# Performance work log

Measured on AMD Instinct MI355X. Metric: run time of the kernel, lower is better.

## Reference

```python
import jax, jax.numpy as jnp
import numpy as np

B, S, L, DM, DP, H, HT, NO = 1, 64, 256, 256, 128, 8, 4, 32
EPS = 1e-5


def _lin(key, din, dout):
    k1, k2 = jax.random.split(key)
    s = 1.0 / np.sqrt(din)
    w = jax.random.uniform(k1, (din, dout), minval=-s, maxval=s, dtype=jnp.float32)
    b = jax.random.uniform(k2, (dout,), minval=-s, maxval=s, dtype=jnp.float32)
    return w, b


def setup_inputs() -> dict:
    key = jax.random.key(0)
    ks = jax.random.split(key, 16)
    inp = {}
    inp['msa'] = jax.random.normal(ks[0], (B, S, L, DM), dtype=jnp.float32)
    inp['pair'] = jax.random.normal(ks[1], (B, L, L, DP), dtype=jnp.float32)
    # row attention
    inp['row_norm_g'] = jnp.ones((DM,), jnp.float32); inp['row_norm_b'] = jnp.zeros((DM,), jnp.float32)
    inp['row_qkv_w'], inp['row_qkv_b'] = _lin(ks[2], DM, 3 * DM)
    inp['row_out_w'], inp['row_out_b'] = _lin(ks[3], DM, DM)
    # column attention
    inp['col_norm_g'] = jnp.ones((DM,), jnp.float32); inp['col_norm_b'] = jnp.zeros((DM,), jnp.float32)
    inp['col_qkv_w'], inp['col_qkv_b'] = _lin(ks[4], DM, 3 * DM)
    inp['col_out_w'], inp['col_out_b'] = _lin(ks[5], DM, DM)
    inp['ff_norm_g'] = jnp.ones((DM,), jnp.float32); inp['ff_norm_b'] = jnp.zeros((DM,), jnp.float32)
    inp['ff_w1'], inp['ff_b1'] = _lin(ks[6], DM, 4 * DM)
    inp['ff_w2'], inp['ff_b2'] = _lin(ks[7], 4 * DM, DM)
    # outer product mean
    inp['op_norm_g'] = jnp.ones((DM,), jnp.float32); inp['op_norm_b'] = jnp.zeros((DM,), jnp.float32)
    inp['op_a_w'], inp['op_a_b'] = _lin(ks[8], DM, NO)
    inp['op_b_w'], inp['op_b_b'] = _lin(ks[9], DM, NO)
    inp['op_out_w'], inp['op_out_b'] = _lin(ks[10], NO * NO, DP)
    # triangle attention
    inp['tri_norm_g'] = jnp.ones((DP,), jnp.float32); inp['tri_norm_b'] = jnp.zeros((DP,), jnp.float32)
    inp['tri_qkv_w'], inp['tri_qkv_b'] = _lin(ks[11], DP, 3 * DP)
    inp['tri_out_w'], inp['tri_out_b'] = _lin(ks[12], DP, DP)
    return inp


def layer_norm(x, g, b):
    m = jnp.mean(x, axis=-1, keepdims=True)
    v = jnp.mean(jnp.square(x - m), axis=-1, keepdims=True)
    return (x - m) * jax.lax.rsqrt(v + EPS) * g + b


def mha(x, qkv_w, qkv_b, out_w, out_b, n_heads):
    # x: (..., n, d); attention over axis n. Dropout is eval-mode (identity).
    *lead, n, d = x.shape
    hd = d // n_heads
    qkv = x @ qkv_w + qkv_b
    q, k, v = jnp.split(qkv, 3, axis=-1)
    q = q.reshape(*lead, n, n_heads, hd)
    k = k.reshape(*lead, n, n_heads, hd)
    v = v.reshape(*lead, n, n_heads, hd)
    attn = jnp.einsum('...ihd,...jhd->...hij', q, k) * (hd ** -0.5)
    attn = jnp.clip(attn, -50.0, 50.0)
    attn = jax.nn.softmax(attn, axis=-1)
    out = jnp.einsum('...hij,...jhd->...ihd', attn, v).reshape(*lead, n, d)
    return out @ out_w + out_b


def reference(msa, pair,
              row_norm_g, row_norm_b, row_qkv_w, row_qkv_b, row_out_w, row_out_b,
              col_norm_g, col_norm_b, col_qkv_w, col_qkv_b, col_out_w, col_out_b,
              ff_norm_g, ff_norm_b, ff_w1, ff_b1, ff_w2, ff_b2,
              op_norm_g, op_norm_b, op_a_w, op_a_b, op_b_w, op_b_b, op_out_w, op_out_b,
              tri_norm_g, tri_norm_b, tri_qkv_w, tri_qkv_b, tri_out_w, tri_out_b):
    # row attention over seq_len axis
    msa = msa + mha(layer_norm(msa, row_norm_g, row_norm_b),
                    row_qkv_w, row_qkv_b, row_out_w, row_out_b, H)
    # column attention: transpose (b s n d) -> (b n s d), attend over n_seqs
    msa_t = jnp.swapaxes(msa, 1, 2)
    msa_t = msa_t + mha(layer_norm(msa_t, col_norm_g, col_norm_b),
                        col_qkv_w, col_qkv_b, col_out_w, col_out_b, H)
    msa = jnp.swapaxes(msa_t, 1, 2)
    # feed-forward
    h = layer_norm(msa, ff_norm_g, ff_norm_b)
    msa = msa + (jax.nn.relu(h @ ff_w1 + ff_b1) @ ff_w2 + ff_b2)
    # outer product mean: msa -> pair update
    m = layer_norm(msa, op_norm_g, op_norm_b)
    a = m @ op_a_w + op_a_b   # (b, s, L, NO)
    b_ = m @ op_b_w + op_b_b  # (b, s, L, NO)
    n_seqs = msa.shape[1]
    outer = jnp.einsum('bsic,bsjd->bijcd', a, b_) / float(n_seqs)  # (b, L, L, NO, NO)
    bsz, Ld = outer.shape[0], outer.shape[1]
    pair = pair + outer.reshape(bsz, Ld, Ld, NO * NO) @ op_out_w + op_out_b
    # triangle attention (row-wise attention over last L axis, 4 heads)
    pn = layer_norm(pair, tri_norm_g, tri_norm_b)
    pair = pair + mha(pn, tri_qkv_w, tri_qkv_b, tri_out_w, tri_out_b, HT)
    return msa, pair
```

## Files before the change

### kernel.cpp

```cpp
#include <hip/hip_runtime.h>
#include <hip/hip_bf16.h>


#define S_ 64
#define L_ 256
#define DM_ 256
#define DP_ 128
#define H_ 8
#define HT_ 4
#define NO_ 32

typedef __hip_bfloat16 bf16;
typedef short short4s __attribute__((ext_vector_type(4)));
typedef short short8 __attribute__((ext_vector_type(8)));
typedef float floatx4 __attribute__((ext_vector_type(4)));

__device__ __forceinline__ short f2bfs(float x) {
  union { float f; unsigned u; } v;
  v.f = x;
  unsigned r = (v.u + 0x7fffu + ((v.u >> 16) & 1u)) >> 16;
  return (short)r;
}

__global__ void k_ln(const float* __restrict__ src, bf16* __restrict__ dst,
                     const float* __restrict__ g, const float* __restrict__ bta, int D) {
  int row = blockIdx.x * 4 + (threadIdx.x >> 6);
  const float* x = src + (size_t)row * D;
  bf16* y = dst + (size_t)row * D;
  int t = threadIdx.x & 63;
  float v[4];
  int cnt = 0;
  float sum = 0.f;
  for (int e = t; e < D; e += 64) { float xv = x[e]; v[cnt++] = xv; sum += xv; }
  #pragma unroll
  for (int o = 32; o; o >>= 1) sum += __shfl_down(sum, o);
  sum = __shfl(sum, 0);
  float mean = sum / D;
  float var = 0.f;
  for (int k = 0; k < cnt; k++) { float d = v[k] - mean; var += d * d; }
  #pragma unroll
  for (int o = 32; o; o >>= 1) var += __shfl_down(var, o);
  var = __shfl(var, 0);
  float rstd = rsqrtf(var / D + 1e-5f);
  cnt = 0;
  for (int e = t; e < D; e += 64)
    y[e] = __float2bfloat16((v[cnt++] - mean) * rstd * g[e] + bta[e]);
}

struct WtJob { const float* W; bf16* Wt; int K; int N; int nblk; };
struct WtJobs { WtJob j[10]; };

__global__ void k_wt_all(WtJobs jobs) {
  __shared__ float tile[32][33];
  int b = blockIdx.x;
  int ji = 0;
  while (ji < 9 && b >= jobs.j[ji].nblk) { b -= jobs.j[ji].nblk; ji++; }
  const float* W = jobs.j[ji].W;
  bf16* Wt = jobs.j[ji].Wt;
  int K = jobs.j[ji].K, N = jobs.j[ji].N;
  int kt = K >> 5;
  int k0 = (b % kt) * 32, n0 = (b / kt) * 32;
  int tid = threadIdx.x;
  for (int e = tid; e < 1024; e += 256) {
    int r = e >> 5, c = e & 31;
    tile[r][c] = W[(size_t)(k0 + r) * N + (n0 + c)];
  }
  __syncthreads();
  for (int e = tid; e < 1024; e += 256) {
    int r = e >> 5, c = e & 31;
    Wt[(size_t)(n0 + r) * K + (k0 + c)] = __float2bfloat16(tile[c][r]);
  }
}

__global__ void k_wtopm(const float* __restrict__ W, bf16* __restrict__ Wt,
                        const float* __restrict__ ba, const float* __restrict__ bb,
                        float* __restrict__ bias_ab) {
  if (blockIdx.x == 0 && threadIdx.x < 64)
    bias_ab[threadIdx.x] = threadIdx.x < 32 ? ba[threadIdx.x] : bb[threadIdx.x - 32];
  int idx = blockIdx.x * 256 + threadIdx.x;
  int d = idx >> 10, kk = idx & 1023;
  int e = kk >> 5, c = kk & 31;
  Wt[idx] = __float2bfloat16(W[(size_t)(c * 32 + e) * 128 + d]);
}

__global__ void k_topm(const bf16* __restrict__ ab, bf16* __restrict__ a_t,
                       bf16* __restrict__ b_t) {
  __shared__ bf16 tile[64][34];
  int i = blockIdx.x;
  int y = blockIdx.y;
  bf16* out = y ? b_t : a_t;
  int tid = threadIdx.x;
  for (int e = tid; e < 64 * 32; e += 256) {
    int s = e >> 5, c = e & 31;
    tile[s][c] = ab[((size_t)s * L_ + i) * 64 + y * 32 + c];
  }
  __syncthreads();
  for (int e = tid; e < 64 * 32; e += 256) {
    int c = e >> 6, s = e & 63;
    out[((size_t)i * NO_ + c) * S_ + s] = tile[s][c];
  }
}

template<int MODE>
__global__ void k_gemm(const bf16* __restrict__ A, const bf16* __restrict__ Wt,
                       const float* __restrict__ bias, float* __restrict__ Cf,
                       bf16* __restrict__ Cb, const float* __restrict__ Csrc,
                       float* __restrict__ Cdup, int M, int N, int K, float scale) {
  __shared__ short As[128 * 64];
  __shared__ short Bs[128 * 64];
  const int tid = threadIdx.x;
  const int nwg = gridDim.x * gridDim.y;
  const int wgid = blockIdx.y * gridDim.x + blockIdx.x;
  const int q = nwg >> 3, r8 = nwg & 7;
  const int xcd = wgid & 7, loc = wgid >> 3;
  const int swz = (xcd < r8 ? xcd * (q + 1) : r8 * (q + 1) + (xcd - r8) * q) + loc;
  const int by = swz / gridDim.x, bx = swz - by * gridDim.x;
  const int m0 = by * 128, n0 = bx * 128;
  const int w = tid >> 6, l = tid & 63;
  const int wm = (w >> 1) * 64, wn = (w & 1) * 64;
  const int lr = l & 15, lk = l >> 4;
  floatx4 acc[4][4] = {};
  const short* Ash = (const short*)A;
  const short* Bsh = (const short*)Wt;
  for (int k0 = 0; k0 < K; k0 += 64) {
    for (int e = tid; e < 1024; e += 256) {
      int r = e >> 3, kg = e & 7;
      short8 v = *(const short8*)(Ash + (size_t)(m0 + r) * K + k0 + kg * 8);
      *(short8*)(&As[r * 64 + ((kg ^ (r & 7)) * 8)]) = v;
    }
    for (int e = tid; e < 1024; e += 256) {
      int r = e >> 3, kg = e & 7;
      int n = n0 + r;
      short8 v = {0, 0, 0, 0, 0, 0, 0, 0};
      if (n < N) v = *(const short8*)(Bsh + (size_t)n * K + k0 + kg * 8);
      *(short8*)(&Bs[r * 64 + ((kg ^ (r & 7)) * 8)]) = v;
    }
    __syncthreads();
    #pragma unroll
    for (int kk = 0; kk < 2; kk++) {
      short8 af[4], bfr[4];
      #pragma unroll
      for (int mi = 0; mi < 4; mi++) {
        int row = wm + mi * 16 + lr;
        int kg = kk * 4 + lk;
        af[mi] = *(const short8*)(&As[row * 64 + ((kg ^ (row & 7)) * 8)]);
      }
      #pragma unroll
      for (int ni = 0; ni < 4; ni++) {
        int row = wn + ni * 16 + lr;
        int kg = kk * 4 + lk;
        bfr[ni] = *(const short8*)(&Bs[row * 64 + ((kg ^ (row & 7)) * 8)]);
      }
      #pragma unroll
      for (int mi = 0; mi < 4; mi++)
        #pragma unroll
        for (int ni = 0; ni < 4; ni++)
          acc[mi][ni] = __builtin_amdgcn_mfma_f32_16x16x32_bf16(af[mi], bfr[ni], acc[mi][ni], 0, 0, 0);
    }
    __syncthreads();
  }
  #pragma unroll
  for (int ni = 0; ni < 4; ni++) {
    int n = n0 + wn + ni * 16 + lr;
    if (n >= N) continue;
    float bv = bias ? bias[n] : 0.f;
    #pragma unroll
    for (int mi = 0; mi < 4; mi++) {
      int mbase = m0 + wm + mi * 16 + lk * 4;
      #pragma unroll
      for (int r = 0; r < 4; r++) {
        float v = acc[mi][ni][r] * scale + bv;
        size_t idx = (size_t)(mbase + r) * N + n;
        if (MODE == 0) Cf[idx] = v;
        else if (MODE == 1) Cf[idx] += v;
        else if (MODE == 2) Cb[idx] = __float2bfloat16(v);
        else if (MODE == 3) Cb[idx] = __float2bfloat16(fmaxf(v, 0.f));
        else if (MODE == 4) Cf[idx] = Csrc[idx] + v;
        else if (MODE == 5) { float t = Cf[idx] + v; Cf[idx] = t; Cdup[idx] = t; }
      }
    }
  }
}

__global__ __launch_bounds__(256) void k_opm_fused(
    const bf16* __restrict__ a_t, const bf16* __restrict__ b_t,
    const bf16* __restrict__ Wt, const float* __restrict__ bias,
    const float* __restrict__ pair_in, float* __restrict__ pair_out) {
  __shared__ short U[32 * 512];
  const int i = blockIdx.y;
  const int jg = blockIdx.x;
  const int tid = threadIdx.x;
  const int w = tid >> 6, l = tid & 63;
  const int lr = l & 15, lk = l >> 4;
  const short* at = (const short*)a_t;
  const short* bt = (const short*)b_t;
  const short* wt = (const short*)Wt;

  short8 af[2][2];
  #pragma unroll
  for (int kh = 0; kh < 2; kh++)
    #pragma unroll
    for (int ks = 0; ks < 2; ks++)
      af[kh][ks] = *(const short8*)(at + ((size_t)i * 32 + kh * 16 + lr) * 64 + ks * 32 + lk * 8);

  floatx4 pacc[2][2] = {};
  #pragma unroll
  for (int kh = 0; kh < 2; kh++) {
    #pragma unroll
    for (int sc = 0; sc < 2; sc++) {
      floatx4 uacc[8] = {};
      const size_t rowbase = ((size_t)(jg * 32 + sc * 16) << 5) + w * 128;
      #pragma unroll
      for (int ks = 0; ks < 2; ks++)
        #pragma unroll
        for (int nt = 0; nt < 8; nt++) {
          short8 bfr = *(const short8*)(bt + (rowbase + nt * 16 + lr) * 64 + ks * 32 + lk * 8);
          uacc[nt] = __builtin_amdgcn_mfma_f32_16x16x32_bf16(af[kh][ks], bfr, uacc[nt], 0, 0, 0);
        }
      #pragma unroll
      for (int nt = 0; nt < 8; nt++) {
        int npos = w * 128 + nt * 16 + lr;
        int jj = sc * 16 + (npos >> 5);
        int e = npos & 31;
        int g = e * 2 + (lk >> 1);
        int off = (lk & 1) * 4;
        short4s pk;
        pk.x = f2bfs(uacc[nt][0] * 0.015625f);
        pk.y = f2bfs(uacc[nt][1] * 0.015625f);
        pk.z = f2bfs(uacc[nt][2] * 0.015625f);
        pk.w = f2bfs(uacc[nt][3] * 0.015625f);
        *(short4s*)(&U[jj * 512 + ((g ^ (jj & 7)) << 3) + off]) = pk;
      }
    }
    __syncthreads();
    #pragma unroll 4
    for (int ks = 0; ks < 16; ks++) {
      short8 afp[2];
      #pragma unroll
      for (int mt = 0; mt < 2; mt++) {
        int row = mt * 16 + lr;
        int g = ks * 4 + lk;
        afp[mt] = *(const short8*)(&U[row * 512 + ((g ^ (row & 7)) << 3)]);
      }
      int wko = (ks * 2 + (lk >> 1)) * 32 + kh * 16 + (lk & 1) * 8;
      #pragma unroll
      for (int ntl = 0; ntl < 2; ntl++) {
        int d = (w * 2 + ntl) * 16 + lr;
        short8 bfr = *(const short8*)(wt + (size_t)d * 1024 + wko);
        #pragma unroll
        for (int mt = 0; mt < 2; mt++)
          pacc[mt][ntl] = __builtin_amdgcn_mfma_f32_16x16x32_bf16(afp[mt], bfr, pacc[mt][ntl], 0, 0, 0);
      }
    }
    __syncthreads();
  }
  int jbase = jg * 32;
  #pragma unroll
  for (int ntl = 0; ntl < 2; ntl++) {
    int d = (w * 2 + ntl) * 16 + lr;
    float bv = bias[d];
    #pragma unroll
    for (int mt = 0; mt < 2; mt++)
      #pragma unroll
      for (int r = 0; r < 4; r++) {
        int j = jbase + mt * 16 + lk * 4 + r;
        size_t idx = ((size_t)i * L_ + j) * DP_ + d;
        pair_out[idx] = pair_in[idx] + pacc[mt][ntl][r] + bv;
      }
  }
}

template<int N>
__global__ __launch_bounds__(256) void k_attn_mfma(
    const bf16* __restrict__ qkv, bf16* __restrict__ out, int dmodel,
    int tokStride, int leadStride, int otokStride, int oleadStride, float scale) {
  constexpr int NT = N / 16;
  constexpr int NK = N / 32;
  constexpr int NIC = N / 64;
  __shared__ short Ks[N * 32];
  __shared__ short Vt[N * 32];
  __shared__ short Qs[2048];
  __shared__ short P[64 * N];

  const int lead = blockIdx.x;
  const int h = blockIdx.y;
  const short* base = (const short*)qkv + (size_t)lead * leadStride;
  const int qoff = h * 32, koff = dmodel + h * 32, voff = 2 * dmodel + h * 32;
  const int tid = threadIdx.x;
  const int l = tid & 63, w = tid >> 6;
  const int lr = l & 15, lk = l >> 4;

  for (int e = tid; e < N * 4; e += 256) {
    int j = e >> 2, kg = e & 3;
    short8 v = *(const short8*)(base + (size_t)j * tokStride + koff + kg * 8);
    *(short8*)(&Ks[(kg * N + j) * 8]) = v;
  }
  for (int e = tid; e < N * 32; e += 256) {
    int j = e >> 5, d = e & 31;
    Vt[((j >> 5) * 4 + ((j >> 3) & 3)) * 256 + d * 8 + (j & 7)] = base[(size_t)j * tokStride + voff + d];
  }
  __syncthreads();

  for (int ic = 0; ic < NIC; ic++) {
    {
      int r = tid >> 2, kg = tid & 3;
      short8 v = *(const short8*)(base + (size_t)(ic * 64 + r) * tokStride + qoff + kg * 8);
      *(short8*)(&Qs[(kg * 64 + r) * 8]) = v;
    }
    short8 aq = *(const short8*)(&Qs[(lk * 64 + w * 16 + lr) * 8]);
    floatx4 sa[NT];
    #pragma unroll
    for (int t = 0; t < NT; t++) {
      short8 bk = *(const short8*)(&Ks[(lk * N + t * 16 + lr) * 8]);
      floatx4 z = {0.f, 0.f, 0.f, 0.f};
      sa[t] = __builtin_amdgcn_mfma_f32_16x16x32_bf16(aq, bk, z, 0, 0, 0);
    }

    float mrow[4] = {-1e30f, -1e30f, -1e30f, -1e30f};
    #pragma unroll
    for (int t = 0; t < NT; t++)
      #pragma unroll
      for (int r = 0; r < 4; r++) {
        float s = fminf(fmaxf(sa[t][r] * scale, -50.f), 50.f);
        sa[t][r] = s;
        mrow[r] = fmaxf(mrow[r], s);
      }
    #pragma unroll
    for (int o = 1; o <= 8; o <<= 1)
      #pragma unroll
      for (int r = 0; r < 4; r++) mrow[r] = fmaxf(mrow[r], __shfl_xor(mrow[r], o));
    float srow[4] = {0.f, 0.f, 0.f, 0.f};
    #pragma unroll
    for (int t = 0; t < NT; t++)
      #pragma unroll
      for (int r = 0; r < 4; r++) {
        float p = __expf(sa[t][r] - mrow[r]);
        sa[t][r] = p;
        srow[r] += p;
      }
    #pragma unroll
    for (int o = 1; o <= 8; o <<= 1)
      #pragma unroll
      for (int r = 0; r < 4; r++) srow[r] += __shfl_xor(srow[r], o);
    float inv[4];
    #pragma unroll
    for (int r = 0; r < 4; r++) inv[r] = 1.f / srow[r];

    #pragma unroll
    for (int t = 0; t < NT; t++) {
      int c = t * 16 + lr;
      int kstep = c >> 5, kslot = (c >> 3) & 3, u = c & 7;
      #pragma unroll
      for (int r = 0; r < 4; r++) {
        int row = w * 16 + lk * 4 + r;
        P[((kstep * 4 + kslot) * 64 + row) * 8 + u] = f2bfs(sa[t][r] * inv[r]);
      }
    }

    floatx4 oacc[2] = {{0.f,0.f,0.f,0.f},{0.f,0.f,0.f,0.f}};
    #pragma unroll
    for (int ks = 0; ks < NK; ks++) {
      short8 ap = *(const short8*)(&P[((ks * 4 + lk) * 64 + w * 16 + lr) * 8]);
      #pragma unroll
      for (int ct = 0; ct < 2; ct++) {
        short8 bv = *(const short8*)(&Vt[((ks * 4 + lk) * 32 + ct * 16 + lr) * 8]);
        oacc[ct] = __builtin_amdgcn_mfma_f32_16x16x32_bf16(ap, bv, oacc[ct], 0, 0, 0);
      }
    }
    bf16* ob = out + (size_t)lead * oleadStride + h * 32;
    #pragma unroll
    for (int ct = 0; ct < 2; ct++)
      #pragma unroll
      for (int r = 0; r < 4; r++) {
        int tok = ic * 64 + w * 16 + lk * 4 + r;
        ob[(size_t)tok * otokStride + ct * 16 + lr] = __float2bfloat16(oacc[ct][r]);
      }
  }
}

extern "C" void kernel_launch(void* const* d_in, const int* in_sizes, int n_in,
                              void* d_out, int out_size, void* d_ws, size_t ws_size,
                              hipStream_t stream) {
  const float* msa_in    = (const float*)d_in[0];
  const float* pair_in   = (const float*)d_in[1];
  const float* row_ng    = (const float*)d_in[2];
  const float* row_nb    = (const float*)d_in[3];
  const float* row_qkv_w = (const float*)d_in[4];
  const float* row_qkv_b = (const float*)d_in[5];
  const float* row_out_w = (const float*)d_in[6];
  const float* row_out_b = (const float*)d_in[7];
  const float* col_ng    = (const float*)d_in[8];
  const float* col_nb    = (const float*)d_in[9];
  const float* col_qkv_w = (const float*)d_in[10];
  const float* col_qkv_b = (const float*)d_in[11];
  const float* col_out_w = (const float*)d_in[12];
  const float* col_out_b = (const float*)d_in[13];
  const float* ff_ng     = (const float*)d_in[14];
  const float* ff_nb     = (const float*)d_in[15];
  const float* ff_w1     = (const float*)d_in[16];
  const float* ff_b1     = (const float*)d_in[17];
  const float* ff_w2     = (const float*)d_in[18];
  const float* ff_b2     = (const float*)d_in[19];
  const float* op_ng     = (const float*)d_in[20];
  const float* op_nb     = (const float*)d_in[21];
  const float* op_a_w    = (const float*)d_in[22];
  const float* op_a_b    = (const float*)d_in[23];
  const float* op_b_w    = (const float*)d_in[24];
  const float* op_b_b    = (const float*)d_in[25];
  const float* op_out_w  = (const float*)d_in[26];
  const float* op_out_b  = (const float*)d_in[27];
  const float* tri_ng    = (const float*)d_in[28];
  const float* tri_nb    = (const float*)d_in[29];
  const float* tri_qkv_w = (const float*)d_in[30];
  const float* tri_qkv_b = (const float*)d_in[31];
  const float* tri_out_w = (const float*)d_in[32];
  const float* tri_out_b = (const float*)d_in[33];

  const int MT = S_ * L_;
  const int PT = L_ * L_;

  char* ws = (char*)d_ws;
  float* msa_f  = (float*)(ws);
  float* pair_f = (float*)(ws + 16777216);
  char*  X      = ws + 50331648;
  bf16*  ln_b   = (bf16*)(ws + 100663296);
  bf16*  ao_b   = (bf16*)(ws + 117440512);
  bf16*  ab_buf = (bf16*)(ws + 134217728);
  bf16*  a_t    = (bf16*)(ws + 136314880);
  bf16*  b_t    = (bf16*)(ws + 137363456);
  bf16*  wts    = (bf16*)(ws + 138412032);
  float* bias_ab = (float*)(ws + 141557760);

  bf16* row_qkv_wt = wts;
  bf16* col_qkv_wt = row_qkv_wt + 196608;
  bf16* row_out_wt = col_qkv_wt + 196608;
  bf16* col_out_wt = row_out_wt + 65536;
  bf16* ff_w1t     = col_out_wt + 65536;
  bf16* ff_w2t     = ff_w1t + 262144;
  bf16* op_ab_wt   = ff_w2t + 262144;
  bf16* op_out_wt  = op_ab_wt + 16384;
  bf16* tri_qkv_wt = op_out_wt + 131072;
  bf16* tri_out_wt = tri_qkv_wt + 49152;

  bf16* qkv_bf = (bf16*)X;
  bf16* ffh    = (bf16*)X;

  float* dout_msa  = (float*)d_out;
  float* dout_pair = (float*)d_out + (size_t)MT * DM_;

  const float scale = 0.17677669529663687f;

  WtJobs jobs;
  jobs.j[0] = {row_qkv_w, row_qkv_wt, 256, 768, 192};
  jobs.j[1] = {col_qkv_w, col_qkv_wt, 256, 768, 192};
  jobs.j[2] = {row_out_w, row_out_wt, 256, 256, 64};
  jobs.j[3] = {col_out_w, col_out_wt, 256, 256, 64};
  jobs.j[4] = {ff_w1, ff_w1t, 256, 1024, 256};
  jobs.j[5] = {ff_w2, ff_w2t, 1024, 256, 256};
  jobs.j[6] = {op_a_w, op_ab_wt, 256, 32, 8};
  jobs.j[7] = {op_b_w, op_ab_wt + 32 * 256, 256, 32, 8};
  jobs.j[8] = {tri_qkv_w, tri_qkv_wt, 128, 384, 48};
  jobs.j[9] = {tri_out_w, tri_out_wt, 128, 128, 16};
  k_wt_all<<<1104, 256, 0, stream>>>(jobs);
  k_wtopm<<<512, 256, 0, stream>>>(op_out_w, op_out_wt, op_a_b, op_b_b, bias_ab);

  k_ln<<<MT / 4, 256, 0, stream>>>(msa_in, ln_b, row_ng, row_nb, DM_);
  k_gemm<2><<<dim3(6, 128), 256, 0, stream>>>(ln_b, row_qkv_wt, row_qkv_b, nullptr, qkv_bf, nullptr, nullptr, MT, 768, 256, 1.f);
  k_attn_mfma<256><<<dim3(S_, H_), 256, 0, stream>>>(qkv_bf, ao_b, DM_, 768, L_ * 768, DM_, L_ * DM_, scale);
  k_gemm<4><<<dim3(2, 128), 256, 0, stream>>>(ao_b, row_out_wt, row_out_b, msa_f, nullptr, msa_in, nullptr, MT, DM_, DM_, 1.f);

  k_ln<<<MT / 4, 256, 0, stream>>>(msa_f, ln_b, col_ng, col_nb, DM_);
  k_gemm<2><<<dim3(6, 128), 256, 0, stream>>>(ln_b, col_qkv_wt, col_qkv_b, nullptr, qkv_bf, nullptr, nullptr, MT, 768, 256, 1.f);
  k_attn_mfma<64><<<dim3(L_, H_), 256, 0, stream>>>(qkv_bf, ao_b, DM_, L_ * 768, 768, L_ * DM_, DM_, scale);
  k_gemm<1><<<dim3(2, 128), 256, 0, stream>>>(ao_b, col_out_wt, col_out_b, msa_f, nullptr, nullptr, nullptr, MT, DM_, DM_, 1.f);

  k_ln<<<MT / 4, 256, 0, stream>>>(msa_f, ln_b, ff_ng, ff_nb, DM_);
  k_gemm<3><<<dim3(8, 128), 256, 0, stream>>>(ln_b, ff_w1t, ff_b1, nullptr, ffh, nullptr, nullptr, MT, 1024, 256, 1.f);
  k_gemm<5><<<dim3(2, 128), 256, 0, stream>>>(ffh, ff_w2t, ff_b2, msa_f, nullptr, nullptr, dout_msa, MT, DM_, 1024, 1.f);

  k_ln<<<MT / 4, 256, 0, stream>>>(msa_f, ln_b, op_ng, op_nb, DM_);
  k_gemm<2><<<dim3(1, 128), 256, 0, stream>>>(ln_b, op_ab_wt, bias_ab, nullptr, ab_buf, nullptr, nullptr, MT, 64, DM_, 1.f);
  k_topm<<<dim3(L_, 2), 256, 0, stream>>>(ab_buf, a_t, b_t);
  k_opm_fused<<<dim3(8, L_), 256, 0, stream>>>(a_t, b_t, op_out_wt, op_out_b, pair_in, pair_f);

  k_ln<<<PT / 4, 256, 0, stream>>>(pair_f, ln_b, tri_ng, tri_nb, DP_);
  k_gemm<2><<<dim3(3, 512), 256, 0, stream>>>(ln_b, tri_qkv_wt, tri_qkv_b, nullptr, qkv_bf, nullptr, nullptr, PT, 384, DP_, 1.f);
  k_attn_mfma<256><<<dim3(L_, HT_), 256, 0, stream>>>(qkv_bf, ao_b, DP_, 384, L_ * 384, DP_, L_ * DP_, scale);
  k_gemm<4><<<dim3(1, 512), 256, 0, stream>>>(ao_b, tri_out_wt, tri_out_b, dout_pair, nullptr, pair_f, nullptr, PT, DP_, DP_, 1.f);
}
```

Baseline: 523.8 us.

## Add 64x64-tile GEMM with XCD swizzle for narrow GEMMs; overlap OPM stages

Adds a k_gemm64 kernel with 64x64 tiles and an XCD-aware block index swizzle. It replaces the original GEMM for the narrow-N GEMMs (out projections, FF2, OPM a/b, tri out) so those launches get more workgroups and fill more compute units. Separately, the OPM fused kernel now computes the second half of U in registers while it runs the projection on the first half, so MFMA work overlaps across the two halves. The cost is a larger register footprint in the OPM kernel, one extra barrier, and smaller tiles with less data reuse per block.

```diff
diff --git a/kernel.cpp b/kernel.cpp
--- a/kernel.cpp
+++ b/kernel.cpp
@@ -182,6 +182,87 @@
   }
 }
 
+template<int MODE>
+__global__ void k_gemm64(const bf16* __restrict__ A, const bf16* __restrict__ Wt,
+                         const float* __restrict__ bias, float* __restrict__ Cf,
+                         bf16* __restrict__ Cb, const float* __restrict__ Csrc,
+                         float* __restrict__ Cdup, int M, int N, int K, float scale) {
+  __shared__ short As[64 * 64];
+  __shared__ short Bs[64 * 64];
+  const int tid = threadIdx.x;
+  const int nwg = gridDim.x * gridDim.y;
+  const int wgid = blockIdx.y * gridDim.x + blockIdx.x;
+  const int q = nwg >> 3, r8 = nwg & 7;
+  const int xcd = wgid & 7, loc = wgid >> 3;
+  const int swz = (xcd < r8 ? xcd * (q + 1) : r8 * (q + 1) + (xcd - r8) * q) + loc;
+  const int by = swz / gridDim.x, bx = swz - by * gridDim.x;
+  const int m0 = by * 64, n0 = bx * 64;
+  const int w = tid >> 6, l = tid & 63;
+  const int wm = (w >> 1) * 32, wn = (w & 1) * 32;
+  const int lr = l & 15, lk = l >> 4;
+  floatx4 acc[2][2] = {};
+  const short* Ash = (const short*)A;
+  const short* Bsh = (const short*)Wt;
+  for (int k0 = 0; k0 < K; k0 += 64) {
+    for (int e = tid; e < 512; e += 256) {
+      int r = e >> 3, kg = e & 7;
+      short8 v = *(const short8*)(Ash + (size_t)(m0 + r) * K + k0 + kg * 8);
+      *(short8*)(&As[r * 64 + ((kg ^ (r & 7)) * 8)]) = v;
+    }
+    for (int e = tid; e < 512; e += 256) {
+      int r = e >> 3, kg = e & 7;
+      int n = n0 + r;
+      short8 v = {0, 0, 0, 0, 0, 0, 0, 0};
+      if (n < N) v = *(const short8*)(Bsh + (size_t)n * K + k0 + kg * 8);
+      *(short8*)(&Bs[r * 64 + ((kg ^ (r & 7)) * 8)]) = v;
+    }
+    __syncthreads();
+    #pragma unroll
+    for (int kk = 0; kk < 2; kk++) {
+      short8 af[2], bfr[2];
+      #pragma unroll
+      for (int mi = 0; mi < 2; mi++) {
+        int row = wm + mi * 16 + lr;
+        int kg = kk * 4 + lk;
+        af[mi] = *(const short8*)(&As[row * 64 + ((kg ^ (row & 7)) * 8)]);
+      }
+      #pragma unroll
+      for (int ni = 0; ni < 2; ni++) {
+        int row = wn + ni * 16 + lr;
+        int kg = kk * 4 + lk;
+        bfr[ni] = *(const short8*)(&Bs[row * 64 + ((kg ^ (row & 7)) * 8)]);
+      }
+      #pragma unroll
+      for (int mi = 0; mi < 2; mi++)
+        #pragma unroll
+        for (int ni = 0; ni < 2; ni++)
+          acc[mi][ni] = __builtin_amdgcn_mfma_f32_16x16x32_bf16(af[mi], bfr[ni], acc[mi][ni], 0, 0, 0);
+    }
+    __syncthreads();
+  }
+  #pragma unroll
+  for (int ni = 0; ni < 2; ni++) {
+    int n = n0 + wn + ni * 16 + lr;
+    if (n >= N) continue;
+    float bv = bias ? bias[n] : 0.f;
+    #pragma unroll
+    for (int mi = 0; mi < 2; mi++) {
+      int mbase = m0 + wm + mi * 16 + lk * 4;
+      #pragma unroll
+      for (int r = 0; r < 4; r++) {
+        float v = acc[mi][ni][r] * scale + bv;
+        size_t idx = (size_t)(mbase + r) * N + n;
+        if (MODE == 0) Cf[idx] = v;
+        else if (MODE == 1) Cf[idx] += v;
+        else if (MODE == 2) Cb[idx] = __float2bfloat16(v);
+        else if (MODE == 3) Cb[idx] = __float2bfloat16(fmaxf(v, 0.f));
+        else if (MODE == 4) Cf[idx] = Csrc[idx] + v;
+        else if (MODE == 5) { float t = Cf[idx] + v; Cf[idx] = t; Cdup[idx] = t; }
+      }
+    }
+  }
+}
+
 __global__ __launch_bounds__(256) void k_opm_fused(
     const bf16* __restrict__ a_t, const bf16* __restrict__ b_t,
     const bf16* __restrict__ Wt, const float* __restrict__ bias,
@@ -204,19 +285,23 @@
       af[kh][ks] = *(const short8*)(at + ((size_t)i * 32 + kh * 16 + lr) * 64 + ks * 32 + lk * 8);
 
   floatx4 pacc[2][2] = {};
-  #pragma unroll
-  for (int kh = 0; kh < 2; kh++) {
+
+  auto computeU = [&](int kh, floatx4 (&ua)[2][8]) {
     #pragma unroll
     for (int sc = 0; sc < 2; sc++) {
-      floatx4 uacc[8] = {};
       const size_t rowbase = ((size_t)(jg * 32 + sc * 16) << 5) + w * 128;
       #pragma unroll
       for (int ks = 0; ks < 2; ks++)
         #pragma unroll
         for (int nt = 0; nt < 8; nt++) {
           short8 bfr = *(const short8*)(bt + (rowbase + nt * 16 + lr) * 64 + ks * 32 + lk * 8);
-          uacc[nt] = __builtin_amdgcn_mfma_f32_16x16x32_bf16(af[kh][ks], bfr, uacc[nt], 0, 0, 0);
+          ua[sc][nt] = __builtin_amdgcn_mfma_f32_16x16x32_bf16(af[kh][ks], bfr, ua[sc][nt], 0, 0, 0);
         }
+    }
+  };
+  auto writeU = [&](floatx4 (&ua)[2][8]) {
+    #pragma unroll
+    for (int sc = 0; sc < 2; sc++)
       #pragma unroll
       for (int nt = 0; nt < 8; nt++) {
         int npos = w * 128 + nt * 16 + lr;
@@ -225,14 +310,14 @@
         int g = e * 2 + (lk >> 1);
         int off = (lk & 1) * 4;
         short4s pk;
-        pk.x = f2bfs(uacc[nt][0] * 0.015625f);
-        pk.y = f2bfs(uacc[nt][1] * 0.015625f);
-        pk.z = f2bfs(uacc[nt][2] * 0.015625f);
-        pk.w = f2bfs(uacc[nt][3] * 0.015625f);
+        pk.x = f2bfs(ua[sc][nt][0] * 0.015625f);
+        pk.y = f2bfs(ua[sc][nt][1] * 0.015625f);
+        pk.z = f2bfs(ua[sc][nt][2] * 0.015625f);
+        pk.w = f2bfs(ua[sc][nt][3] * 0.015625f);
         *(short4s*)(&U[jj * 512 + ((g ^ (jj & 7)) << 3) + off]) = pk;
       }
-    }
-    __syncthreads();
+  };
+  auto proj = [&](int kh) {
     #pragma unroll 4
     for (int ks = 0; ks < 16; ks++) {
       short8 afp[2];
@@ -252,8 +337,20 @@
           pacc[mt][ntl] = __builtin_amdgcn_mfma_f32_16x16x32_bf16(afp[mt], bfr, pacc[mt][ntl], 0, 0, 0);
       }
     }
-    __syncthreads();
-  }
+  };
+
+  floatx4 ua[2][8] = {};
+  computeU(0, ua);
+  writeU(ua);
+  __syncthreads();
+  floatx4 ub[2][8] = {};
+  computeU(1, ub);
+  proj(0);
+  __syncthreads();
+  writeU(ub);
+  __syncthreads();
+  proj(1);
+
   int jbase = jg * 32;
   #pragma unroll
   for (int ntl = 0; ntl < 2; ntl++) {
@@ -467,24 +564,24 @@
   k_ln<<<MT / 4, 256, 0, stream>>>(msa_in, ln_b, row_ng, row_nb, DM_);
   k_gemm<2><<<dim3(6, 128), 256, 0, stream>>>(ln_b, row_qkv_wt, row_qkv_b, nullptr, qkv_bf, nullptr, nullptr, MT, 768, 256, 1.f);
   k_attn_mfma<256><<<dim3(S_, H_), 256, 0, stream>>>(qkv_bf, ao_b, DM_, 768, L_ * 768, DM_, L_ * DM_, scale);
-  k_gemm<4><<<dim3(2, 128), 256, 0, stream>>>(ao_b, row_out_wt, row_out_b, msa_f, nullptr, msa_in, nullptr, MT, DM_, DM_, 1.f);
+  k_gemm64<4><<<dim3(4, 256), 256, 0, stream>>>(ao_b, row_out_wt, row_out_b, msa_f, nullptr, msa_in, nullptr, MT, DM_, DM_, 1.f);
 
   k_ln<<<MT / 4, 256, 0, stream>>>(msa_f, ln_b, col_ng, col_nb, DM_);
   k_gemm<2><<<dim3(6, 128), 256, 0, stream>>>(ln_b, col_qkv_wt, col_qkv_b, nullptr, qkv_bf, nullptr, nullptr, MT, 768, 256, 1.f);
   k_attn_mfma<64><<<dim3(L_, H_), 256, 0, stream>>>(qkv_bf, ao_b, DM_, L_ * 768, 768, L_ * DM_, DM_, scale);
-  k_gemm<1><<<dim3(2, 128), 256, 0, stream>>>(ao_b, col_out_wt, col_out_b, msa_f, nullptr, nullptr, nullptr, MT, DM_, DM_, 1.f);
+  k_gemm64<1><<<dim3(4, 256), 256, 0, stream>>>(ao_b, col_out_wt, col_out_b, msa_f, nullptr, nullptr, nullptr, MT, DM_, DM_, 1.f);
 
   k_ln<<<MT / 4, 256, 0, stream>>>(msa_f, ln_b, ff_ng, ff_nb, DM_);
   k_gemm<3><<<dim3(8, 128), 256, 0, stream>>>(ln_b, ff_w1t, ff_b1, nullptr, ffh, nullptr, nullptr, MT, 1024, 256, 1.f);
-  k_gemm<5><<<dim3(2, 128), 256, 0, stream>>>(ffh, ff_w2t, ff_b2, msa_f, nullptr, nullptr, dout_msa, MT, DM_, 1024, 1.f);
+  k_gemm64<5><<<dim3(4, 256), 256, 0, stream>>>(ffh, ff_w2t, ff_b2, msa_f, nullptr, nullptr, dout_msa, MT, DM_, 1024, 1.f);
 
   k_ln<<<MT / 4, 256, 0, stream>>>(msa_f, ln_b, op_ng, op_nb, DM_);
-  k_gemm<2><<<dim3(1, 128), 256, 0, stream>>>(ln_b, op_ab_wt, bias_ab, nullptr, ab_buf, nullptr, nullptr, MT, 64, DM_, 1.f);
+  k_gemm64<2><<<dim3(1, 256), 256, 0, stream>>>(ln_b, op_ab_wt, bias_ab, nullptr, ab_buf, nullptr, nullptr, MT, 64, DM_, 1.f);
   k_topm<<<dim3(L_, 2), 256, 0, stream>>>(ab_buf, a_t, b_t);
   k_opm_fused<<<dim3(8, L_), 256, 0, stream>>>(a_t, b_t, op_out_wt, op_out_b, pair_in, pair_f);
 
   k_ln<<<PT / 4, 256, 0, stream>>>(pair_f, ln_b, tri_ng, tri_nb, DP_);
   k_gemm<2><<<dim3(3, 512), 256, 0, stream>>>(ln_b, tri_qkv_wt, tri_qkv_b, nullptr, qkv_bf, nullptr, nullptr, PT, 384, DP_, 1.f);
   k_attn_mfma<256><<<dim3(L_, HT_), 256, 0, stream>>>(qkv_bf, ao_b, DP_, 384, L_ * 384, DP_, L_ * DP_, scale);
-  k_gemm<4><<<dim3(1, 512), 256, 0, stream>>>(ao_b, tri_out_wt, tri_out_b, dout_pair, nullptr, pair_f, nullptr, PT, DP_, DP_, 1.f);
-}
+  k_gemm64<4><<<dim3(2, 1024), 256, 0, stream>>>(ao_b, tri_out_wt, tri_out_b, dout_pair, nullptr, pair_f, nullptr, PT, DP_, DP_, 1.f);
+}
```

After: 484.0 us. 7.6% less time.
